# Performance work log

Measured on AMD Instinct MI355X. Metric: run time of the kernel, lower is better.

The kernel has to match this reference:

```python
import jax, jax.numpy as jnp
import numpy as np

NORM_EPS = 1e-6
QK_SCALE = 1.0 / 128.0  # 1/d_head (muP)
ROTARY_BASE = 10000
INFTY_APPROX = 1e30

B, T, M, H, D = 2, 2048, 1024, 8, 128


def _rmsnorm(x, eps=NORM_EPS):
    # normalize over the last (head) dim; no learned gains (norm_gains=False)
    ms = jnp.mean(jnp.square(x), axis=-1, keepdims=True)
    return x / jnp.sqrt(ms + eps)


def _rope(x, base=ROTARY_BASE):
    # x: [b, h, t, d]; rotate (even-half, odd-half) pairs as in the source
    length, width = x.shape[-2], x.shape[-1]
    half = width // 2
    pos = jnp.arange(length, dtype=x.dtype)[:, None]            # [t, 1]
    freqs = jnp.power(jnp.asarray(base, x.dtype), -jnp.arange(half, dtype=x.dtype) / half)[None, :]
    rad = pos * freqs                                            # [t, half]
    cos = jnp.cos(rad)[None, None]
    sin = jnp.sin(rad)[None, None]
    even, odd = jnp.split(x, 2, axis=-1)
    return jnp.concatenate([even * cos - odd * sin, even * sin + odd * cos], axis=-1)


def setup_inputs() -> dict:
    key = jax.random.key(0)
    ks = jax.random.split(key, 5)
    std = M ** -0.5
    return {
        "x": jax.random.normal(ks[0], (B, T, M), jnp.float32),
        "wq": jax.random.normal(ks[1], (M, H, D), jnp.float32) * std,
        "wk": jax.random.normal(ks[2], (M, H, D), jnp.float32) * std,
        "wv": jax.random.normal(ks[3], (M, H, D), jnp.float32) * std,
        "wo": jax.random.normal(ks[4], (H, D, M), jnp.float32) * std,
    }


def reference(x, wq, wk, wv, wo):
    # projections: [b, h, t, d]
    q = jnp.einsum('bim,mhd->bhid', x, wq)
    k = jnp.einsum('bim,mhd->bhid', x, wk)
    v = jnp.einsum('bim,mhd->bhid', x, wv)
    # qk RMSNorm (norm_gains=False)
    q = _rmsnorm(q)
    k = _rmsnorm(k)
    # inline RoPE
    q = _rope(q)
    k = _rope(k)
    # scaled scores: mult applied to both q and k (mult^2 = qk_scale)
    mult = jnp.asarray(QK_SCALE ** 0.5, q.dtype)
    s = jnp.einsum('bhid,bhjd->bhij', q * mult, k * mult)
    # causal mask: subtract large constant where i < j
    t = s.shape[-1]
    mask = (jnp.arange(t)[:, None] < jnp.arange(t)[None, :]).astype(s.dtype)
    s = s - jnp.asarray(INFTY_APPROX, s.dtype) * mask[None, None]
    p = jax.nn.softmax(s, axis=-1)
    o = jnp.einsum('bhij,bhjd->bhid', p, v)
    return jnp.einsum('bhid,hdm->bim', o, wo)
```

## Files before the change

kernel.cpp:

```cpp
#include <hip/hip_runtime.h>
#include <hip/hip_bf16.h>
#include <math.h>

#define B_  2
#define T_  2048
#define M_  1024
#define H_  8
#define D_  128
#define NROW (B_ * T_)
#define HD  (H_ * D_)

#define NORM_EPS 1e-6f
#define QK_MULT  0.08838834764831845f
#define LN_BASE_64 0.14391156510f

typedef short bf16x8  __attribute__((ext_vector_type(8)));
typedef float f32x4   __attribute__((ext_vector_type(4)));
typedef float f32x16  __attribute__((ext_vector_type(16)));
typedef unsigned int uint32x2 __attribute__((ext_vector_type(2)));

static __device__ __forceinline__ unsigned short f2bf(float f) {
    union { __hip_bfloat16 h; unsigned short u; } cv;
    cv.h = __float2bfloat16(f);
    return cv.u;
}
static __device__ __forceinline__ unsigned int pk2bf(float a, float b) {
    return ((unsigned int)f2bf(b) << 16) | f2bf(a);
}

static __device__ __forceinline__ void gload_lds16(const unsigned short* g,
                                                   unsigned short* l) {
    __builtin_amdgcn_global_load_lds(
        (const __attribute__((address_space(1))) void*)g,
        (__attribute__((address_space(3))) void*)l, 16, 0, 0);
}

__global__ __launch_bounds__(256) void prep(const float* __restrict__ x,
                                            const float* __restrict__ w0,
                                            const float* __restrict__ w1,
                                            const float* __restrict__ w2,
                                            const float* __restrict__ w3,
                                            unsigned short* __restrict__ xb,
                                            unsigned short* __restrict__ wqkvT,
                                            unsigned short* __restrict__ woT)
{
    __shared__ float t[32][33];
    const int z = blockIdx.z;
    if (z == 4) {
        const size_t base = ((size_t)blockIdx.y * 32 + blockIdx.x) * 4096;
        #pragma unroll
        for (int it = 0; it < 4; ++it) {
            const size_t i = base + it * 1024 + threadIdx.x * 4;
            const float4 v = *(const float4*)(x + i);
            ushort4 o;
            o.x = f2bf(v.x); o.y = f2bf(v.y); o.z = f2bf(v.z); o.w = f2bf(v.w);
            *(ushort4*)(xb + i) = o;
        }
        return;
    }
    const float* in = z == 0 ? w0 : (z == 1 ? w1 : (z == 2 ? w2 : w3));
    unsigned short* out = z < 3 ? (wqkvT + (size_t)z * 1024 * 1024) : woT;

    const int tx = threadIdx.x & 31;
    const int ty = threadIdx.x >> 5;
    const int n0 = blockIdx.x * 32;
    const int k0 = blockIdx.y * 32;
    #pragma unroll
    for (int r = 0; r < 4; ++r)
        t[ty + r * 8][tx] = in[(size_t)(k0 + ty + r * 8) * 1024 + n0 + tx];
    __syncthreads();
    #pragma unroll
    for (int r = 0; r < 4; ++r)
        out[(size_t)(n0 + ty + r * 8) * 1024 + k0 + tx] = f2bf(t[tx][ty + r * 8]);
}

__global__ __launch_bounds__(256) void gemm_qkv(const unsigned short* __restrict__ A,
                                                const unsigned short* __restrict__ Bt,
                                                unsigned short* __restrict__ oq,
                                                unsigned short* __restrict__ ok,
                                                unsigned short* __restrict__ vt)
{
    __shared__ __align__(16) unsigned short smem[17408];
    #define AsQ(buf) (smem + (buf) * 4096)
    #define BsQ(buf) (smem + 8192 + (buf) * 4096)

    const int tid  = threadIdx.x;
    const int lane = tid & 63;
    const int w    = tid >> 6;
    const int g    = lane >> 4;
    const int lc   = lane & 15;

    const int m0 = blockIdx.y * 128;
    const int n0 = blockIdx.x * 128;

    const unsigned short* aBase = A  + (size_t)m0 * 1024;
    const unsigned short* bBase = Bt + (size_t)n0 * 1024;

    int dstOff[2];
    size_t srcOff[2];
    #pragma unroll
    for (int it = 0; it < 2; ++it) {
        const int u  = tid + it * 256;
        const int r2 = u >> 2;
        const int sg = (u & 3) ^ (r2 & 3);
        dstOff[it] = u * 8;
        srcOff[it] = (size_t)r2 * 1024 + sg * 8;
    }

    f32x4 acc[2][8];
    #pragma unroll
    for (int i = 0; i < 2; ++i)
        #pragma unroll
        for (int j = 0; j < 8; ++j)
            acc[i][j] = (f32x4){0.f, 0.f, 0.f, 0.f};

    #pragma unroll
    for (int it = 0; it < 2; ++it) {
        gload_lds16(aBase + srcOff[it], AsQ(0) + dstOff[it]);
        gload_lds16(bBase + srcOff[it], BsQ(0) + dstOff[it]);
    }

    for (int kt = 0; kt < 32; ++kt) {
        const int cur = kt & 1;
        __syncthreads();

        if (kt < 31) {
            const int k0n = (kt + 1) * 32;
            #pragma unroll
            for (int it = 0; it < 2; ++it) {
                gload_lds16(aBase + srcOff[it] + k0n, AsQ(cur ^ 1) + dstOff[it]);
                gload_lds16(bBase + srcOff[it] + k0n, BsQ(cur ^ 1) + dstOff[it]);
            }
        }

        const int sw = (g ^ (lc & 3)) << 3;
        bf16x8 af[2], bfr[8];
        #pragma unroll
        for (int i = 0; i < 2; ++i)
            af[i] = *(const bf16x8*)&AsQ(cur)[(w * 32 + i * 16 + lc) * 32 + sw];
        #pragma unroll
        for (int j = 0; j < 8; ++j)
            bfr[j] = *(const bf16x8*)&BsQ(cur)[(j * 16 + lc) * 32 + sw];

        #pragma unroll
        for (int i = 0; i < 2; ++i)
            #pragma unroll
            for (int j = 0; j < 8; ++j)
                acc[i][j] = __builtin_amdgcn_mfma_f32_16x16x32_bf16(af[i], bfr[j], acc[i][j], 0, 0, 0);
    }

    const int which = n0 >> 10;
    const int ncol0 = n0 & 1023;
    if (which < 2) {
        unsigned short* outp = which == 0 ? oq : ok;
        float freq[4];
        #pragma unroll
        for (int j = 0; j < 4; ++j)
            freq[j] = __expf(-(float)(j * 16 + lc) * LN_BASE_64);

        #pragma unroll
        for (int i = 0; i < 2; ++i)
            #pragma unroll
            for (int r = 0; r < 4; ++r) {
                float s = 0.f;
                #pragma unroll
                for (int j = 0; j < 8; ++j) s += acc[i][j][r] * acc[i][j][r];
                #pragma unroll
                for (int off = 1; off < 16; off <<= 1) s += __shfl_xor(s, off);
                const float rms = rsqrtf(s * (1.0f / 128.0f) + NORM_EPS) * QK_MULT;

                const int trow = m0 + w * 32 + i * 16 + g * 4 + r;
                const float tpos = (float)(trow & (T_ - 1));
                unsigned short* op = outp + (size_t)trow * 1024 + ncol0;
                #pragma unroll
                for (int j = 0; j < 4; ++j) {
                    float sn, cs;
                    __sincosf(tpos * freq[j], &sn, &cs);
                    const float e = acc[i][j][r] * rms;
                    const float o = acc[i][j + 4][r] * rms;
                    op[j * 16 + lc]      = f2bf(e * cs - o * sn);
                    op[j * 16 + lc + 64] = f2bf(e * sn + o * cs);
                }
            }
    } else {
        const int b2 = m0 >> 11;
        const int hh = ncol0 >> 7;
        const int PAD = 136;
        __syncthreads();
        #pragma unroll
        for (int i = 0; i < 2; ++i) {
            const int t0 = w * 32 + i * 16 + g * 4;
            #pragma unroll
            for (int j = 0; j < 8; ++j) {
                uint2 val;
                val.x = pk2bf(acc[i][j][0], acc[i][j][1]);
                val.y = pk2bf(acc[i][j][2], acc[i][j][3]);
                *(uint2*)&smem[(j * 16 + lc) * PAD + t0] = val;
            }
        }
        __syncthreads();
        const int row  = tid >> 1;
        const int half = tid & 1;
        const unsigned short* src = &smem[row * PAD + half * 64];
        unsigned short* dst = vt + ((size_t)(b2 * 8 + hh) * 128 + row) * T_
                                 + (m0 & 2047) + half * 64;
        #pragma unroll
        for (int it2 = 0; it2 < 8; ++it2)
            *(uint4*)(dst + it2 * 8) = *(const uint4*)(src + it2 * 8);
    }
    #undef AsQ
    #undef BsQ
}

__global__ __launch_bounds__(256) void gemm_out(const unsigned short* __restrict__ A,
                                                const unsigned short* __restrict__ Bt,
                                                float* __restrict__ cf)
{
    __shared__ unsigned short As[2][128 * 64];
    __shared__ unsigned short Bs[2][64 * 64];

    const int tid  = threadIdx.x;
    const int lane = tid & 63;
    const int w    = tid >> 6;
    const int g    = lane >> 4;
    const int lc   = lane & 15;
    const int wm   = w >> 1;
    const int wn   = w & 1;

    const int m0 = blockIdx.y * 128;
    const int n0 = blockIdx.x * 64;

    const unsigned short* aBase = A  + (size_t)m0 * 1024;
    const unsigned short* bBase = Bt + (size_t)n0 * 1024;

    int dstA[4], dstB[2];
    size_t srcA[4], srcB[2];
    #pragma unroll
    for (int it = 0; it < 4; ++it) {
        const int u  = tid + it * 256;
        const int r2 = u >> 3;
        const int sg = (u & 7) ^ (r2 & 7);
        dstA[it] = u * 8;
        srcA[it] = (size_t)r2 * 1024 + sg * 8;
    }
    #pragma unroll
    for (int it = 0; it < 2; ++it) {
        const int u  = tid + it * 256;
        const int r2 = u >> 3;
        const int sg = (u & 7) ^ (r2 & 7);
        dstB[it] = u * 8;
        srcB[it] = (size_t)r2 * 1024 + sg * 8;
    }

    f32x4 acc[4][2];
    #pragma unroll
    for (int i = 0; i < 4; ++i)
        #pragma unroll
        for (int j = 0; j < 2; ++j)
            acc[i][j] = (f32x4){0.f, 0.f, 0.f, 0.f};

    #pragma unroll
    for (int it = 0; it < 4; ++it)
        gload_lds16(aBase + srcA[it], &As[0][dstA[it]]);
    #pragma unroll
    for (int it = 0; it < 2; ++it)
        gload_lds16(bBase + srcB[it], &Bs[0][dstB[it]]);

    for (int kt = 0; kt < 16; ++kt) {
        const int cur = kt & 1;
        __syncthreads();

        if (kt < 15) {
            const int k0n = (kt + 1) * 64;
            #pragma unroll
            for (int it = 0; it < 4; ++it)
                gload_lds16(aBase + srcA[it] + k0n, &As[cur ^ 1][dstA[it]]);
            #pragma unroll
            for (int it = 0; it < 2; ++it)
                gload_lds16(bBase + srcB[it] + k0n, &Bs[cur ^ 1][dstB[it]]);
        }

        #pragma unroll
        for (int dc = 0; dc < 2; ++dc) {
            const int sw = ((dc * 4 + g) ^ (lc & 7)) << 3;
            bf16x8 af[4], bfr[2];
            #pragma unroll
            for (int i = 0; i < 4; ++i)
                af[i] = *(const bf16x8*)&As[cur][(wm * 64 + i * 16 + lc) * 64 + sw];
            #pragma unroll
            for (int j = 0; j < 2; ++j)
                bfr[j] = *(const bf16x8*)&Bs[cur][(wn * 32 + j * 16 + lc) * 64 + sw];

            #pragma unroll
            for (int i = 0; i < 4; ++i)
                #pragma unroll
                for (int j = 0; j < 2; ++j)
                    acc[i][j] = __builtin_amdgcn_mfma_f32_16x16x32_bf16(af[i], bfr[j], acc[i][j], 0, 0, 0);
        }
    }

    #pragma unroll
    for (int i = 0; i < 4; ++i) {
        const int mrow = m0 + wm * 64 + i * 16 + g * 4;
        #pragma unroll
        for (int j = 0; j < 2; ++j) {
            const int nc = n0 + wn * 32 + j * 16 + lc;
            #pragma unroll
            for (int r = 0; r < 4; ++r)
                cf[(size_t)(mrow + r) * 1024 + nc] = acc[i][j][r];
        }
    }
}

__global__ __launch_bounds__(256) void flash_attn(const unsigned short* __restrict__ qb,
                                                  const unsigned short* __restrict__ kb,
                                                  const unsigned short* __restrict__ vt,
                                                  unsigned short* __restrict__ o)
{
    __shared__ __align__(16) unsigned short smem[4 * 16384 + 128];
    float* lscr = (float*)(smem + 4 * 16384);

    const int tid  = threadIdx.x;
    const int lane = tid & 63;
    const int w    = tid >> 6;
    const int wj   = w >> 1;
    const int wq2  = w & 1;
    const int qcol = lane & 31;
    const int hi   = lane >> 5;

    const int bid = blockIdx.x;
    const int s   = bid >> 3;
    const int bh  = (bid & 7) + 8 * (s & 1);
    const int qtA = s >> 1;
    const int qtB = 31 - qtA;
    const int h   = bh & (H_ - 1);
    const int b   = bh >> 3;

    const size_t bhbase  = (size_t)b * T_ * HD + (size_t)h * 128;
    const size_t bhvbase = (size_t)bh * 128 * T_;

    int mI[4];
    size_t srcKoff[4], srcVoff[4];
    #pragma unroll
    for (int it = 0; it < 4; ++it) {
        const int m = (w * 4 + it) * 64 + lane;
        mI[it] = m;
        const int jK = m >> 4, cK = (m & 15) ^ (jK & 15);
        srcKoff[it] = (size_t)jK * 1024 + cK * 8;
        const int dV = m >> 3, cV = (m & 7) ^ (dV & 7);
        srcVoff[it] = (size_t)dV * T_ + cV * 8;
    }
    const unsigned short* kgb = kb + bhbase;
    const unsigned short* vgb = vt + bhvbase;

#define SRCU(s_) ((s_) > qtA ? (s_) - qtA - 1 : (s_))
#define STAGE(js_, bf_) {                                                    \
        const size_t jo = (size_t)(js_) * 64;                                \
        unsigned short* Kd = smem + (bf_) * 16384;                           \
        unsigned short* Vd = Kd + 8192;                                      \
        _Pragma("unroll")                                                    \
        for (int it = 0; it < 4; ++it)                                       \
            gload_lds16(kgb + jo * 1024 + srcKoff[it], &Kd[mI[it] * 8]);     \
        _Pragma("unroll")                                                    \
        for (int it = 0; it < 4; ++it)                                       \
            gload_lds16(vgb + jo + srcVoff[it], &Vd[mI[it] * 8]);            \
    }

    bf16x8 qf[8];
    {
        const unsigned short* qp = qb + bhbase
            + (size_t)(qtA * 64 + wq2 * 32 + qcol) * 1024 + hi * 8;
        #pragma unroll
        for (int ks = 0; ks < 8; ++ks)
            qf[ks] = *(const bf16x8*)(qp + ks * 16);
    }

    float lsum = 0.f;
    f32x16 otacc[4];
    #pragma unroll
    for (int dch = 0; dch < 4; ++dch)
        #pragma unroll
        for (int r = 0; r < 16; ++r) otacc[dch][r] = 0.f;

    STAGE(SRCU(0), 0);
    STAGE(SRCU(1), 1);
    STAGE(SRCU(2), 2);

    for (int u = 0; u < 33; ++u) {
        asm volatile("s_waitcnt vmcnt(16)" ::: "memory");
        __builtin_amdgcn_s_barrier();
        {
            const int sn = u + 3 <= 32 ? u + 3 : 32;
            STAGE(SRCU(sn), (u + 3) & 3);
        }

        unsigned short* Ks = smem + (u & 3) * 16384;
        unsigned short* Vs = Ks + 8192;

        const bool atD  = (u == qtA) || (u == 32);
        const bool dead = atD && (wj > wq2);
        if (!dead) {
            const int jrow = wj * 32 + qcol;

            bf16x8 kf[8], vf[8];
            #pragma unroll
            for (int ks = 0; ks < 8; ++ks) {
                const int c = ks * 2 + hi;
                kf[ks] = *(const bf16x8*)&Ks[(jrow * 16 + (c ^ (lane & 15))) * 8];
            }
            #pragma unroll
            for (int ks2 = 0; ks2 < 2; ++ks2)
                #pragma unroll
                for (int dch = 0; dch < 4; ++dch) {
                    const int c = wj * 4 + ks2 * 2 + hi;
                    const int drow = dch * 32 + qcol;
                    vf[ks2 * 4 + dch] = *(const bf16x8*)&Vs[(drow * 8 + (c ^ (lane & 7))) * 8];
                }

            f32x16 sacc0, sacc1;
            #pragma unroll
            for (int r = 0; r < 16; ++r) { sacc0[r] = 0.f; sacc1[r] = 0.f; }
            __builtin_amdgcn_s_setprio(1);
            #pragma unroll
            for (int ks = 0; ks < 8; ks += 2) {
                sacc0 = __builtin_amdgcn_mfma_f32_32x32x16_bf16(kf[ks], qf[ks], sacc0, 0, 0, 0);
                sacc1 = __builtin_amdgcn_mfma_f32_32x32x16_bf16(kf[ks + 1], qf[ks + 1], sacc1, 0, 0, 0);
            }
            __builtin_amdgcn_s_setprio(0);
            f32x16 sacc = sacc0 + sacc1;

            if (atD && wj == wq2) {
                #pragma unroll
                for (int r = 0; r < 16; ++r) {
                    const int jl = (r & 3) + 8 * (r >> 2) + 4 * hi;
                    if (qcol < jl) sacc[r] = -1e30f;
                }
            }

            unsigned int dw[8];
            #pragma unroll
            for (int m2 = 0; m2 < 8; ++m2) {
                const float p0 = __expf(sacc[2 * m2]);
                const float p1 = __expf(sacc[2 * m2 + 1]);
                lsum += p0 + p1;
                dw[m2] = pk2bf(p0, p1);
            }

            __builtin_amdgcn_s_setprio(1);
            #pragma unroll
            for (int ks2 = 0; ks2 < 2; ++ks2) {
                const uint32x2 s02 = __builtin_amdgcn_permlane32_swap(
                    dw[4 * ks2 + 0], dw[4 * ks2 + 2], 0, 0);
                const uint32x2 s13 = __builtin_amdgcn_permlane32_swap(
                    dw[4 * ks2 + 1], dw[4 * ks2 + 3], 0, 0);
                union { unsigned int u2[4]; bf16x8 v; } pf;
                pf.u2[0] = s02[0];
                pf.u2[1] = s13[0];
                pf.u2[2] = s02[1];
                pf.u2[3] = s13[1];
                #pragma unroll
                for (int dch = 0; dch < 4; ++dch)
                    otacc[dch] = __builtin_amdgcn_mfma_f32_32x32x16_bf16(vf[ks2 * 4 + dch], pf.v, otacc[dch], 0, 0, 0);
            }
            __builtin_amdgcn_s_setprio(0);
        }

        if (u == qtA) {
            float* scr = (float*)(smem + (u & 3) * 16384);
            lsum += __shfl_xor(lsum, 32);
            __syncthreads();
            const int row = wq2 * 32 + qcol;
            if (wj == 1) {
                float* s0 = scr + (size_t)row * 128;
                #pragma unroll
                for (int dch = 0; dch < 4; ++dch)
                    #pragma unroll
                    for (int r = 0; r < 16; ++r)
                        s0[dch * 32 + (r & 3) + 8 * (r >> 2) + 4 * hi] = otacc[dch][r];
                if (hi == 0) lscr[row] = lsum;
            }
            __syncthreads();
            if (wj == 0) {
                const float l = lsum + lscr[row];
                const float inv = 1.0f / l;
                const float* s0 = scr + (size_t)row * 128;
                unsigned short* op = o + bhbase + (size_t)(qtA * 64 + row) * 1024;
                #pragma unroll
                for (int dch = 0; dch < 4; ++dch)
                    #pragma unroll
                    for (int k4 = 0; k4 < 4; ++k4) {
                        const int d0 = dch * 32 + 8 * k4 + 4 * hi;
                        const float f0 = (otacc[dch][4 * k4 + 0] + s0[d0 + 0]) * inv;
                        const float f1 = (otacc[dch][4 * k4 + 1] + s0[d0 + 1]) * inv;
                        const float f2 = (otacc[dch][4 * k4 + 2] + s0[d0 + 2]) * inv;
                        const float f3 = (otacc[dch][4 * k4 + 3] + s0[d0 + 3]) * inv;
                        uint2 val;
                        val.x = pk2bf(f0, f1);
                        val.y = pk2bf(f2, f3);
                        *(uint2*)(op + d0) = val;
                    }
            }
            lsum = 0.f;
            #pragma unroll
            for (int dch = 0; dch < 4; ++dch)
                #pragma unroll
                for (int r = 0; r < 16; ++r) otacc[dch][r] = 0.f;
            const unsigned short* qp = qb + bhbase
                + (size_t)(qtB * 64 + wq2 * 32 + qcol) * 1024 + hi * 8;
            #pragma unroll
            for (int ks = 0; ks < 8; ++ks)
                qf[ks] = *(const bf16x8*)(qp + ks * 16);
        }
    }

    {
        float* scr = (float*)smem;
        lsum += __shfl_xor(lsum, 32);
        __syncthreads();
        const int row = wq2 * 32 + qcol;
        if (wj == 1) {
            float* s0 = scr + (size_t)row * 128;
            #pragma unroll
            for (int dch = 0; dch < 4; ++dch)
                #pragma unroll
                for (int r = 0; r < 16; ++r)
                    s0[dch * 32 + (r & 3) + 8 * (r >> 2) + 4 * hi] = otacc[dch][r];
            if (hi == 0) lscr[row] = lsum;
        }
        __syncthreads();
        if (wj == 0) {
            const float l = lsum + lscr[row];
            const float inv = 1.0f / l;
            const float* s0 = scr + (size_t)row * 128;
            unsigned short* op = o + bhbase + (size_t)(qtB * 64 + row) * 1024;
            #pragma unroll
            for (int dch = 0; dch < 4; ++dch)
                #pragma unroll
                for (int k4 = 0; k4 < 4; ++k4) {
                    const int d0 = dch * 32 + 8 * k4 + 4 * hi;
                    const float f0 = (otacc[dch][4 * k4 + 0] + s0[d0 + 0]) * inv;
                    const float f1 = (otacc[dch][4 * k4 + 1] + s0[d0 + 1]) * inv;
                    const float f2 = (otacc[dch][4 * k4 + 2] + s0[d0 + 2]) * inv;
                    const float f3 = (otacc[dch][4 * k4 + 3] + s0[d0 + 3]) * inv;
                    uint2 val;
                    val.x = pk2bf(f0, f1);
                    val.y = pk2bf(f2, f3);
                    *(uint2*)(op + d0) = val;
                }
        }
    }
#undef STAGE
#undef SRCU
}

extern "C" void kernel_launch(void* const* d_in, const int* in_sizes, int n_in,
                              void* d_out, int out_size, void* d_ws, size_t ws_size,
                              hipStream_t stream)
{
    const float* x  = (const float*)d_in[0];
    const float* wq = (const float*)d_in[1];
    const float* wk = (const float*)d_in[2];
    const float* wv = (const float*)d_in[3];
    const float* wo = (const float*)d_in[4];
    float* out = (float*)d_out;

    const size_t SZ = (size_t)NROW * HD;
    unsigned short* qb    = (unsigned short*)d_ws;
    unsigned short* kb    = qb + SZ;
    unsigned short* vt    = kb + SZ;
    unsigned short* ob    = vt + SZ;
    unsigned short* xb    = ob + SZ;
    unsigned short* wqkvT = xb + SZ;
    unsigned short* woT   = wqkvT + 3 * 1024 * 1024;

    prep<<<dim3(32, 32, 5), 256, 0, stream>>>(x, wq, wk, wv, wo, xb, wqkvT, woT);

    gemm_qkv<<<dim3(24, 32), 256, 0, stream>>>(xb, wqkvT, qb, kb, vt);

    flash_attn<<<dim3(256), 256, 0, stream>>>(qb, kb, vt, ob);

    gemm_out<<<dim3(16, 32), 256, 0, stream>>>(ob, woT, out);
}
```

Measured before the change: 191.0 us.

## Split flash-attention KV sweep across two 256-thread groups in a 512-thread block

Doubles the attention block to 512 threads. Two wave groups each process half of the 33-step key/value sweep, one group covering the first query tile's range and the second the rest of the second tile. Each group uses its own double-buffered LDS region, and the final partial outputs and row sums from four slabs are reduced through padded LDS scratch. This halves the serial loop length per block and increases waves in flight, at the cost of more barriers, a larger cross-group reduction and fewer pipeline stages per group (two instead of four).

```diff
diff --git a/kernel.cpp b/kernel.cpp
--- a/kernel.cpp
+++ b/kernel.cpp
@@ -312,21 +312,24 @@
     }
 }
 
-__global__ __launch_bounds__(256) void flash_attn(const unsigned short* __restrict__ qb,
+__global__ __launch_bounds__(512) void flash_attn(const unsigned short* __restrict__ qb,
                                                   const unsigned short* __restrict__ kb,
                                                   const unsigned short* __restrict__ vt,
                                                   unsigned short* __restrict__ o)
 {
-    __shared__ __align__(16) unsigned short smem[4 * 16384 + 128];
-    float* lscr = (float*)(smem + 4 * 16384);
+    __shared__ __align__(16) unsigned short smem[65536 + 512];
+    float* lscrA = (float*)(smem + 65536);
+    float* lscrB = lscrA + 64;
 
     const int tid  = threadIdx.x;
     const int lane = tid & 63;
     const int w    = tid >> 6;
-    const int wj   = w >> 1;
+    const int g2   = w >> 2;
+    const int wj   = (w >> 1) & 1;
     const int wq2  = w & 1;
     const int qcol = lane & 31;
     const int hi   = lane >> 5;
+    const int gtid = tid & 255;
 
     const int bid = blockIdx.x;
     const int s   = bid >> 3;
@@ -343,7 +346,7 @@
     size_t srcKoff[4], srcVoff[4];
     #pragma unroll
     for (int it = 0; it < 4; ++it) {
-        const int m = (w * 4 + it) * 64 + lane;
+        const int m = (((gtid >> 6) * 4 + it)) * 64 + (gtid & 63);
         mI[it] = m;
         const int jK = m >> 4, cK = (m & 15) ^ (jK & 15);
         srcKoff[it] = (size_t)jK * 1024 + cK * 8;
@@ -352,11 +355,12 @@
     }
     const unsigned short* kgb = kb + bhbase;
     const unsigned short* vgb = vt + bhvbase;
-
-#define SRCU(s_) ((s_) > qtA ? (s_) - qtA - 1 : (s_))
-#define STAGE(js_, bf_) {                                                    \
-        const size_t jo = (size_t)(js_) * 64;                                \
-        unsigned short* Kd = smem + (bf_) * 16384;                           \
+    unsigned short* gbase = smem + g2 * 32768;
+
+#define SRCU(p_) ((p_) > qtA ? (p_) - qtA - 1 : (p_))
+#define STAGE(p_, l_) {                                                      \
+        const size_t jo = (size_t)SRCU(p_) * 64;                             \
+        unsigned short* Kd = gbase + ((l_) & 1) * 16384;                     \
         unsigned short* Vd = Kd + 8192;                                      \
         _Pragma("unroll")                                                    \
         for (int it = 0; it < 4; ++it)                                       \
@@ -368,8 +372,9 @@
 
     bf16x8 qf[8];
     {
+        const int qt0 = g2 ? qtB : qtA;
         const unsigned short* qp = qb + bhbase
-            + (size_t)(qtA * 64 + wq2 * 32 + qcol) * 1024 + hi * 8;
+            + (size_t)(qt0 * 64 + wq2 * 32 + qcol) * 1024 + hi * 8;
         #pragma unroll
         for (int ks = 0; ks < 8; ++ks)
             qf[ks] = *(const bf16x8*)(qp + ks * 16);
@@ -382,24 +387,20 @@
         #pragma unroll
         for (int r = 0; r < 16; ++r) otacc[dch][r] = 0.f;
 
-    STAGE(SRCU(0), 0);
-    STAGE(SRCU(1), 1);
-    STAGE(SRCU(2), 2);
-
-    for (int u = 0; u < 33; ++u) {
-        asm volatile("s_waitcnt vmcnt(16)" ::: "memory");
+    STAGE(g2 * 17 + 0, 0);
+    STAGE(g2 ? 18 : 1, 1);
+
+    for (int u = 0; u < 17; ++u) {
+        if (u < 16) asm volatile("s_waitcnt vmcnt(8)" ::: "memory");
+        else        asm volatile("s_waitcnt vmcnt(0)" ::: "memory");
         __builtin_amdgcn_s_barrier();
-        {
-            const int sn = u + 3 <= 32 ? u + 3 : 32;
-            STAGE(SRCU(sn), (u + 3) & 3);
-        }
-
-        unsigned short* Ks = smem + (u & 3) * 16384;
-        unsigned short* Vs = Ks + 8192;
-
-        const bool atD  = (u == qtA) || (u == 32);
-        const bool dead = atD && (wj > wq2);
-        if (!dead) {
+
+        const int p = u + g2 * 17;
+        const bool livep = (p <= 32);
+        const bool atD = (p == qtA) || (p == 32);
+        if (livep && !(atD && (wj > wq2))) {
+            unsigned short* Ks = gbase + (u & 1) * 16384;
+            unsigned short* Vs = Ks + 8192;
             const int jrow = wj * 32 + qcol;
 
             bf16x8 kf[8], vf[8];
@@ -466,85 +467,104 @@
         }
 
         if (u == qtA) {
-            float* scr = (float*)(smem + (u & 3) * 16384);
-            lsum += __shfl_xor(lsum, 32);
-            __syncthreads();
+            float* scrA = (float*)(smem + (qtA & 1) * 16384);
+            float lsA = 0.f;
+            if (g2 == 0) { lsA = lsum + __shfl_xor(lsum, 32); }
+            asm volatile("s_waitcnt lgkmcnt(0)" ::: "memory");
+            __builtin_amdgcn_s_barrier();
             const int row = wq2 * 32 + qcol;
-            if (wj == 1) {
-                float* s0 = scr + (size_t)row * 128;
+            if (g2 == 0 && wj == 1) {
+                float* s0 = scrA + (size_t)row * 128;
                 #pragma unroll
                 for (int dch = 0; dch < 4; ++dch)
                     #pragma unroll
-                    for (int r = 0; r < 16; ++r)
-                        s0[dch * 32 + (r & 3) + 8 * (r >> 2) + 4 * hi] = otacc[dch][r];
-                if (hi == 0) lscr[row] = lsum;
-            }
-            __syncthreads();
-            if (wj == 0) {
-                const float l = lsum + lscr[row];
-                const float inv = 1.0f / l;
-                const float* s0 = scr + (size_t)row * 128;
-                unsigned short* op = o + bhbase + (size_t)(qtA * 64 + row) * 1024;
+                    for (int r = 0; r < 16; ++r) {
+                        const int d = dch * 32 + (r & 3) + 8 * (r >> 2) + 4 * hi;
+                        s0[(d + row) & 127] = otacc[dch][r];
+                    }
+                if (hi == 0) lscrA[row] = lsA;
+            }
+            asm volatile("s_waitcnt lgkmcnt(0)" ::: "memory");
+            __builtin_amdgcn_s_barrier();
+            if (g2 == 0) {
+                if (wj == 0) {
+                    const float l = lsA + lscrA[row];
+                    const float inv = 1.0f / l;
+                    const float* s0 = scrA + (size_t)row * 128;
+                    unsigned short* op = o + bhbase + (size_t)(qtA * 64 + row) * 1024;
+                    #pragma unroll
+                    for (int dch = 0; dch < 4; ++dch)
+                        #pragma unroll
+                        for (int k4 = 0; k4 < 4; ++k4) {
+                            const int d0 = dch * 32 + 8 * k4 + 4 * hi;
+                            const float f0 = (otacc[dch][4 * k4 + 0] + s0[(d0 + 0 + row) & 127]) * inv;
+                            const float f1 = (otacc[dch][4 * k4 + 1] + s0[(d0 + 1 + row) & 127]) * inv;
+                            const float f2 = (otacc[dch][4 * k4 + 2] + s0[(d0 + 2 + row) & 127]) * inv;
+                            const float f3 = (otacc[dch][4 * k4 + 3] + s0[(d0 + 3 + row) & 127]) * inv;
+                            uint2 val;
+                            val.x = pk2bf(f0, f1);
+                            val.y = pk2bf(f2, f3);
+                            *(uint2*)(op + d0) = val;
+                        }
+                }
+                lsum = 0.f;
                 #pragma unroll
                 for (int dch = 0; dch < 4; ++dch)
                     #pragma unroll
-                    for (int k4 = 0; k4 < 4; ++k4) {
-                        const int d0 = dch * 32 + 8 * k4 + 4 * hi;
-                        const float f0 = (otacc[dch][4 * k4 + 0] + s0[d0 + 0]) * inv;
-                        const float f1 = (otacc[dch][4 * k4 + 1] + s0[d0 + 1]) * inv;
-                        const float f2 = (otacc[dch][4 * k4 + 2] + s0[d0 + 2]) * inv;
-                        const float f3 = (otacc[dch][4 * k4 + 3] + s0[d0 + 3]) * inv;
-                        uint2 val;
-                        val.x = pk2bf(f0, f1);
-                        val.y = pk2bf(f2, f3);
-                        *(uint2*)(op + d0) = val;
-                    }
-            }
-            lsum = 0.f;
-            #pragma unroll
-            for (int dch = 0; dch < 4; ++dch)
-                #pragma unroll
-                for (int r = 0; r < 16; ++r) otacc[dch][r] = 0.f;
-            const unsigned short* qp = qb + bhbase
-                + (size_t)(qtB * 64 + wq2 * 32 + qcol) * 1024 + hi * 8;
-            #pragma unroll
-            for (int ks = 0; ks < 8; ++ks)
-                qf[ks] = *(const bf16x8*)(qp + ks * 16);
+                    for (int r = 0; r < 16; ++r) otacc[dch][r] = 0.f;
+                const unsigned short* qp = qb + bhbase
+                    + (size_t)(qtB * 64 + wq2 * 32 + qcol) * 1024 + hi * 8;
+                #pragma unroll
+                for (int ks = 0; ks < 8; ++ks)
+                    qf[ks] = *(const bf16x8*)(qp + ks * 16);
+            }
+        }
+
+        __builtin_amdgcn_s_barrier();
+        const int ln = u + 2;
+        if (ln <= 16) {
+            const int pp = g2 ? (ln + 17 > 32 ? 32 : ln + 17) : ln;
+            STAGE(pp, ln);
         }
     }
 
     {
-        float* scr = (float*)smem;
         lsum += __shfl_xor(lsum, 32);
-        __syncthreads();
-        const int row = wq2 * 32 + qcol;
-        if (wj == 1) {
-            float* s0 = scr + (size_t)row * 128;
+        asm volatile("s_waitcnt lgkmcnt(0)" ::: "memory");
+        __builtin_amdgcn_s_barrier();
+        const int row  = wq2 * 32 + qcol;
+        const int slab = g2 * 2 + wj;
+        float* scrB = (float*)smem;
+        if (slab > 0) {
+            float* s0 = scrB + (size_t)(slab - 1) * (64 * 129) + (size_t)row * 129;
             #pragma unroll
             for (int dch = 0; dch < 4; ++dch)
                 #pragma unroll
                 for (int r = 0; r < 16; ++r)
                     s0[dch * 32 + (r & 3) + 8 * (r >> 2) + 4 * hi] = otacc[dch][r];
-            if (hi == 0) lscr[row] = lsum;
-        }
-        __syncthreads();
-        if (wj == 0) {
-            const float l = lsum + lscr[row];
+            if (hi == 0) lscrB[(slab - 1) * 64 + row] = lsum;
+        }
+        asm volatile("s_waitcnt lgkmcnt(0)" ::: "memory");
+        __builtin_amdgcn_s_barrier();
+        if (slab == 0) {
+            const float l = lsum + lscrB[row] + lscrB[64 + row] + lscrB[128 + row];
             const float inv = 1.0f / l;
-            const float* s0 = scr + (size_t)row * 128;
+            const float* s1 = scrB + (size_t)row * 129;
+            const float* s2 = s1 + 64 * 129;
+            const float* s3 = s2 + 64 * 129;
             unsigned short* op = o + bhbase + (size_t)(qtB * 64 + row) * 1024;
             #pragma unroll
             for (int dch = 0; dch < 4; ++dch)
                 #pragma unroll
                 for (int k4 = 0; k4 < 4; ++k4) {
                     const int d0 = dch * 32 + 8 * k4 + 4 * hi;
-                    const float f0 = (otacc[dch][4 * k4 + 0] + s0[d0 + 0]) * inv;
-                    const float f1 = (otacc[dch][4 * k4 + 1] + s0[d0 + 1]) * inv;
-                    const float f2 = (otacc[dch][4 * k4 + 2] + s0[d0 + 2]) * inv;
-                    const float f3 = (otacc[dch][4 * k4 + 3] + s0[d0 + 3]) * inv;
+                    float f[4];
+                    #pragma unroll
+                    for (int i = 0; i < 4; ++i)
+                        f[i] = (otacc[dch][4 * k4 + i] + s1[d0 + i] + s2[d0 + i] + s3[d0 + i]) * inv;
                     uint2 val;
-                    val.x = pk2bf(f0, f1);
-                    val.y = pk2bf(f2, f3);
+                    val.x = pk2bf(f[0], f[1]);
+                    val.y = pk2bf(f[2], f[3]);
                     *(uint2*)(op + d0) = val;
                 }
         }
@@ -577,7 +597,7 @@
 
     gemm_qkv<<<dim3(24, 32), 256, 0, stream>>>(xb, wqkvT, qb, kb, vt);
 
-    flash_attn<<<dim3(256), 256, 0, stream>>>(qb, kb, vt, ob);
+    flash_attn<<<dim3(256), 512, 0, stream>>>(qb, kb, vt, ob);
 
     gemm_out<<<dim3(16, 32), 256, 0, stream>>>(ob, woT, out);
 }
```

New measurement: 187.7 us. No clear change (-1.7%).
